# Kernel tuning notes

Measured on AMD Instinct MI355X. Metric: run time of the kernel, lower is better.

Reference implementation:

```python
import jax, jax.numpy as jnp
import numpy as np

EPS = 1e-8
ELASTICITY = jnp.array([0.05, 0.12, 0.08, 0.15, 0.10], dtype=jnp.float32)
N_SIDE = 3  # sqrt(control_points=9)


def _kernel_distance(d2):
    # kornia TPS radial basis: 0.5 * r^2 * log(r^2 + eps)
    return 0.5 * d2 * jnp.log(d2 + EPS)


def _pair_sq_dist(a, b):  # [B,N,2],[B,M,2] -> [B,N,M]
    return jnp.sum((a[:, :, None, :] - b[:, None, :, :]) ** 2, axis=-1)


def grid_sample_bilinear(img, grid):
    """F.grid_sample, mode=bilinear, padding_mode=zeros, align_corners=True.
    img [B,C,H,W], grid [B,H,W,2] with (x,y) in [-1,1]."""
    B, C, H, W = img.shape
    gx = (grid[..., 0] + 1.0) * 0.5 * (W - 1)
    gy = (grid[..., 1] + 1.0) * 0.5 * (H - 1)
    x0 = jnp.floor(gx); y0 = jnp.floor(gy)
    x1 = x0 + 1.0; y1 = y0 + 1.0
    wx1 = gx - x0; wx0 = 1.0 - wx1
    wy1 = gy - y0; wy0 = 1.0 - wy1
    b = jnp.arange(B)[:, None, None]

    def gather(yi, xi):
        valid = (xi >= 0) & (xi <= W - 1) & (yi >= 0) & (yi <= H - 1)
        xc = jnp.clip(xi, 0, W - 1).astype(jnp.int32)
        yc = jnp.clip(yi, 0, H - 1).astype(jnp.int32)
        v = img[b, :, yc, xc]  # [B,H,W,C]
        return v * valid[..., None].astype(img.dtype)

    out = (gather(y0, x0) * (wy0 * wx0)[..., None]
           + gather(y0, x1) * (wy0 * wx1)[..., None]
           + gather(y1, x0) * (wy1 * wx0)[..., None]
           + gather(y1, x1) * (wy1 * wx1)[..., None])
    return jnp.transpose(out, (0, 3, 1, 2))


def control_points_src(B):
    ii, jj = jnp.meshgrid(jnp.arange(N_SIDE, dtype=jnp.float32),
                          jnp.arange(N_SIDE, dtype=jnp.float32), indexing='ij')
    src = jnp.stack([2.0 * ii / (N_SIDE - 1) - 1.0,
                     2.0 * jj / (N_SIDE - 1) - 1.0], axis=-1).reshape(-1, 2)
    return jnp.broadcast_to(src, (B, N_SIDE * N_SIDE, 2))


def point_elasticity(masks_f):
    # masks_f [B,nc,H,W]; 5x5 window around each control point, argmax class
    H, W = masks_f.shape[2], masks_f.shape[3]
    elas = []
    for i in range(N_SIDE):
        for j in range(N_SIDE):
            y = int(i / (N_SIDE - 1) * (H - 1))
            x = int(j / (N_SIDE - 1) * (W - 1))
            y0, y1 = max(0, y - 2), min(H, y + 3)
            x0, x1 = max(0, x - 2), min(W, x + 3)
            region = masks_f[:, :, y0:y1, x0:x1].sum((2, 3))  # [B,nc]
            dom = jnp.argmax(region, axis=1)
            elas.append(ELASTICITY[dom])
    return jnp.stack(elas, axis=1)  # [B,9]


def get_tps_transform(src, dst):
    B, N, _ = src.shape
    K = _kernel_distance(_pair_sq_dist(src, src))                 # [B,N,N]
    P = jnp.concatenate([jnp.ones((B, N, 1), src.dtype), src], -1)  # [B,N,3]
    top = jnp.concatenate([K, P], axis=-1)
    bot = jnp.concatenate([jnp.swapaxes(P, 1, 2),
                           jnp.zeros((B, 3, 3), src.dtype)], axis=-1)
    L = jnp.concatenate([top, bot], axis=1)                        # [B,N+3,N+3]
    rhs = jnp.concatenate([dst, jnp.zeros((B, 3, 2), src.dtype)], axis=1)
    w = jnp.linalg.solve(L, rhs)
    return w[:, :N], w[:, N:]


def warp_image_tps(img, centers, kernel_w, affine_w):
    B, C, H, W = img.shape
    gx, gy = jnp.meshgrid(jnp.linspace(-1.0, 1.0, W), jnp.linspace(-1.0, 1.0, H))
    pts = jnp.stack([gx.ravel(), gy.ravel()], axis=-1)             # [HW,2]
    pts = jnp.broadcast_to(pts, (B, H * W, 2))
    k = _kernel_distance(_pair_sq_dist(pts, centers))              # [B,HW,N]
    pts_aug = jnp.concatenate([jnp.ones((B, H * W, 1), img.dtype), pts], -1)
    warped = k @ kernel_w + pts_aug @ affine_w                     # [B,HW,2]
    return grid_sample_bilinear(img, warped.reshape(B, H, W, 2))


def tps_transform(img, masks_f, noise):
    B = img.shape[0]
    disp = noise * point_elasticity(masks_f)[..., None]            # [B,9,2]
    # smooth the single interior control point (i=j=1 -> idx 4)
    neigh = (disp[:, 1] + disp[:, 7] + disp[:, 3] + disp[:, 5]) * 0.25
    disp = disp.at[:, 4].set(0.8 * disp[:, 4] + 0.2 * neigh)
    src = control_points_src(B)
    kw, aw = get_tps_transform(src, src + disp)
    return warp_image_tps(img, src, kw, aw)


def class_aware_mixup(x, masks_f, lam, perm):
    bg = (masks_f.sum(1, keepdims=True) == 0).astype(x.dtype)
    fg = (masks_f == 1).astype(x.dtype).sum(1, keepdims=True)
    return bg * x + fg * (lam * x + (1.0 - lam) * x[perm])


def setup_inputs() -> dict:
    key = jax.random.key(0)
    k1, k2, k3, k4, k5, k6 = jax.random.split(key, 6)
    B, H, W, NC = 128, 192, 192, 5
    return {
        'x': jax.random.normal(k1, (B, 1, H, W), dtype=jnp.float32),
        'masks': jax.random.randint(k2, (B, NC, H, W), 0, 2, dtype=jnp.int32),
        'lam': jax.random.beta(k3, 0.4, 0.4, dtype=jnp.float32),
        'perm': jax.random.permutation(k4, B).astype(jnp.int32),
        'noise_g': jax.random.normal(k5, (B, 9, 2), dtype=jnp.float32),
        'noise_l': jax.random.normal(k6, (B, 9, 2), dtype=jnp.float32),
        'epoch': 10,
        'total_epochs': 100,
    }


def reference(x, masks, lam, perm, noise_g, noise_l, epoch, total_epochs):
    masks_f = masks.astype(x.dtype)
    mixed_x = class_aware_mixup(x, masks_f, lam, perm)
    global_aug = tps_transform(mixed_x, masks_f, noise_g)
    local_aug = tps_transform(x, masks_f, noise_l)
    return (global_aug, local_aug)
```

## Files before the change

kernel.cpp:

```cpp
#include <hip/hip_runtime.h>
#include <math.h>

#define B_   128
#define H_   192
#define W_   192
#define NC_  5
#define HW_  (H_*W_)
#define NPTS 9
#define EPS_ 1e-8f
#define CHUNK 16

typedef int   vint4   __attribute__((ext_vector_type(4)));
typedef float vfloat4 __attribute__((ext_vector_type(4)));
typedef float vfloat2 __attribute__((ext_vector_type(2)));

struct LinvT { float m[12][NPTS]; };

__global__ __launch_bounds__(256) void mixup_kernel(
    const float* __restrict__ x, const int* __restrict__ masks,
    const float* __restrict__ lam_p, const int* __restrict__ perm,
    float* __restrict__ mixed)
{
    int idx = blockIdx.x * 256 + threadIdx.x;
    const int total4 = B_ * HW_ / 4;
    if (idx >= total4) return;
    float lam = lam_p[0];
    int b  = idx / (HW_ / 4);
    int p4 = (idx - b * (HW_ / 4)) * 4;
    const vfloat4 xv = *reinterpret_cast<const vfloat4*>(x + (size_t)b * HW_ + p4);
    int pb = perm[b];
    const vfloat4 xp = *reinterpret_cast<const vfloat4*>(x + (size_t)pb * HW_ + p4);

    vint4 ma[NC_];
    #pragma unroll
    for (int c = 0; c < NC_; ++c) {
        const vint4* mp = reinterpret_cast<const vint4*>(masks + ((size_t)b * NC_ + c) * HW_ + p4);
        ma[c] = __builtin_nontemporal_load(mp);
    }
    vfloat4 outv;
    #pragma unroll
    for (int l = 0; l < 4; ++l) {
        int s = 0, fg = 0;
        #pragma unroll
        for (int c = 0; c < NC_; ++c) { int m = ma[c][l]; s += m; fg += (m == 1); }
        float bg = (s == 0) ? 1.f : 0.f;
        outv[l] = bg * xv[l] + (float)fg * (lam * xv[l] + (1.f - lam) * xp[l]);
    }
    *reinterpret_cast<vfloat4*>(mixed + (size_t)b * HW_ + p4) = outv;
}

__global__ void prep_kernel(const int* __restrict__ masks,
                            const float* __restrict__ ng,
                            const float* __restrict__ nl,
                            LinvT Linv, float* __restrict__ wts)
{
    const float ETAB[5] = {0.05f, 0.12f, 0.08f, 0.15f, 0.1f};
    __shared__ int   sums[NPTS][NC_];
    __shared__ float elas_s[NPTS];
    int b = blockIdx.x;
    int t = threadIdx.x;

    if (t < NPTS * NC_) {
        int pt = t / NC_, c = t - pt * NC_;
        int i = pt / 3, j = pt % 3;
        int yc = (i * (H_ - 1)) / 2;
        int xc = (j * (W_ - 1)) / 2;
        int y0 = yc - 2 < 0 ? 0 : yc - 2;
        int y1 = yc + 3 > H_ ? H_ : yc + 3;
        int x0 = xc - 2 < 0 ? 0 : xc - 2;
        int x1 = xc + 3 > W_ ? W_ : xc + 3;
        int s = 0;
        for (int y = y0; y < y1; ++y)
            for (int xx = x0; xx < x1; ++xx)
                s += masks[((size_t)b * NC_ + c) * HW_ + y * W_ + xx];
        sums[pt][c] = s;
    }
    __syncthreads();
    if (t < NPTS) {
        int best = -1, best_c = 0;
        #pragma unroll
        for (int c = 0; c < NC_; ++c) {
            int s = sums[t][c];
            if (s > best) { best = s; best_c = c; }
        }
        elas_s[t] = ETAB[best_c];
    }
    __syncthreads();
    if (t < 24) {
        int tr = t / 12, r = t - tr * 12;
        const float* noise = (tr == 0) ? ng : nl;
        float disp[NPTS][2];
        #pragma unroll
        for (int k = 0; k < NPTS; ++k) {
            float e = elas_s[k];
            disp[k][0] = noise[((size_t)b * NPTS + k) * 2 + 0] * e;
            disp[k][1] = noise[((size_t)b * NPTS + k) * 2 + 1] * e;
        }
        #pragma unroll
        for (int c = 0; c < 2; ++c) {
            float nb = (disp[1][c] + disp[7][c] + disp[3][c] + disp[5][c]) * 0.25f;
            disp[4][c] = 0.8f * disp[4][c] + 0.2f * nb;
        }
        float a0 = 0.f, a1 = 0.f;
        #pragma unroll
        for (int k = 0; k < NPTS; ++k) {
            float d0 = (float)(k / 3 - 1) + disp[k][0];
            float d1 = (float)(k % 3 - 1) + disp[k][1];
            a0 += Linv.m[r][k] * d0;
            a1 += Linv.m[r][k] * d1;
        }
        float* wout = wts + ((size_t)tr * B_ + b) * 24;
        wout[r * 2 + 0] = a0;
        wout[r * 2 + 1] = a1;
    }
}

__device__ __forceinline__ void tps_coords_pk(
    const vfloat2* __restrict__ wt2, float px, float py, const float* __restrict__ u,
    int& o00, int& o01, int& o10, int& o11,
    float& w00, float& w01, float& w10, float& w11)
{
    vfloat2 g = wt2[9];
    g = __builtin_elementwise_fma((vfloat2){px, px}, wt2[10], g);
    g = __builtin_elementwise_fma((vfloat2){py, py}, wt2[11], g);
    #pragma unroll
    for (int k = 0; k < NPTS; ++k)
        g = __builtin_elementwise_fma((vfloat2){u[k], u[k]}, wt2[k], g);

    const float sc = 0.5f * (float)(W_ - 1);
    float ix = fmaf(g.x, sc, sc);
    float iy = fmaf(g.y, sc, sc);
    float x0f = floorf(ix), y0f = floorf(iy);
    float wx1 = ix - x0f, wx0 = 1.f - wx1;
    float wy1 = iy - y0f, wy0 = 1.f - wy1;
    int x0 = (int)x0f, y0 = (int)y0f;
    float fx0 = ((unsigned)x0 < 192u)       ? wx0 : 0.f;
    float fx1 = ((unsigned)(x0 + 1) < 192u) ? wx1 : 0.f;
    float fy0 = ((unsigned)y0 < 192u)       ? wy0 : 0.f;
    float fy1 = ((unsigned)(y0 + 1) < 192u) ? wy1 : 0.f;
    w00 = fy0 * fx0; w01 = fy0 * fx1; w10 = fy1 * fx0; w11 = fy1 * fx1;
    int o = y0 * W_ + x0;
    o00 = min(max(o, 0), HW_ - 1);
    o01 = min(max(o + 1, 0), HW_ - 1);
    o10 = min(max(o + W_, 0), HW_ - 1);
    o11 = min(max(o + W_ + 1, 0), HW_ - 1);
}

__global__ __launch_bounds__(256, 2) void warp_kernel(
    const float* __restrict__ x, const float* __restrict__ mixed,
    const float* __restrict__ wts, float* __restrict__ out)
{
    int tx  = threadIdx.x;
    int wpx = blockIdx.x * 64 + (tx & 63);
    int h   = blockIdx.y * 4 + (tx >> 6);
    int p   = h * W_ + wpx;
    float px = -1.f + wpx * (2.f / (float)(W_ - 1));
    float py = -1.f + h   * (2.f / (float)(H_ - 1));

    float u[NPTS];
    #pragma unroll
    for (int k = 0; k < NPTS; ++k) {
        float dx = px - (float)(k / 3 - 1);
        float dy = py - (float)(k % 3 - 1);
        float d2 = dx * dx + dy * dy;
        u[k] = 0.5f * d2 * __logf(d2 + EPS_);
    }

    const vfloat2* wt2base = reinterpret_cast<const vfloat2*>(wts);

    #pragma unroll
    for (int g4 = 0; g4 < CHUNK; g4 += 4) {
        int   o00[4], o01[4], o10[4], o11[4];
        float w00[4], w01[4], w10[4], w11[4];
        const float* src[4];
        #pragma unroll
        for (int q = 0; q < 4; ++q) {
            int combo = blockIdx.z * CHUNK + g4 + q;
            int t = combo >> 7;
            int b = combo & (B_ - 1);
            src[q] = (t == 0 ? mixed : x) + (size_t)b * HW_;
            tps_coords_pk(wt2base + (size_t)combo * 12, px, py, u,
                          o00[q], o01[q], o10[q], o11[q],
                          w00[q], w01[q], w10[q], w11[q]);
        }
        float v00[4], v01[4], v10[4], v11[4];
        #pragma unroll
        for (int q = 0; q < 4; ++q) {
            v00[q] = src[q][o00[q]];
            v01[q] = src[q][o01[q]];
            v10[q] = src[q][o10[q]];
            v11[q] = src[q][o11[q]];
        }
        #pragma unroll
        for (int q = 0; q < 4; ++q) {
            int combo = blockIdx.z * CHUNK + g4 + q;
            float val = w00[q] * v00[q] + w01[q] * v01[q] +
                        w10[q] * v10[q] + w11[q] * v11[q];
            __builtin_nontemporal_store(val, &out[(size_t)combo * HW_ + p]);
        }
    }
}

static void build_linv(LinvT* out)
{
    double srcp[NPTS][2];
    for (int k = 0; k < NPTS; ++k) {
        srcp[k][0] = (double)(k / 3) - 1.0;
        srcp[k][1] = (double)(k % 3) - 1.0;
    }
    double A[12][24];
    for (int r = 0; r < 12; ++r)
        for (int c = 0; c < 24; ++c) A[r][c] = 0.0;
    for (int i = 0; i < NPTS; ++i) {
        for (int j = 0; j < NPTS; ++j) {
            double dx = srcp[i][0] - srcp[j][0];
            double dy = srcp[i][1] - srcp[j][1];
            double d2 = dx * dx + dy * dy;
            A[i][j] = 0.5 * d2 * log(d2 + 1e-8);
        }
        A[i][9]  = 1.0; A[i][10] = srcp[i][0]; A[i][11] = srcp[i][1];
        A[9][i]  = 1.0; A[10][i] = srcp[i][0]; A[11][i] = srcp[i][1];
    }
    for (int r = 0; r < 12; ++r) A[r][12 + r] = 1.0;
    for (int col = 0; col < 12; ++col) {
        int piv = col; double mx = fabs(A[col][col]);
        for (int r = col + 1; r < 12; ++r)
            if (fabs(A[r][col]) > mx) { mx = fabs(A[r][col]); piv = r; }
        if (piv != col)
            for (int c = 0; c < 24; ++c) { double tmp = A[col][c]; A[col][c] = A[piv][c]; A[piv][c] = tmp; }
        double d = A[col][col];
        for (int c = 0; c < 24; ++c) A[col][c] /= d;
        for (int r = 0; r < 12; ++r) {
            if (r == col) continue;
            double f = A[r][col];
            if (f != 0.0)
                for (int c = 0; c < 24; ++c) A[r][c] -= f * A[col][c];
        }
    }
    for (int r = 0; r < 12; ++r)
        for (int k = 0; k < NPTS; ++k)
            out->m[r][k] = (float)A[r][12 + k];
}

extern "C" void kernel_launch(void* const* d_in, const int* in_sizes, int n_in,
                              void* d_out, int out_size, void* d_ws, size_t ws_size,
                              hipStream_t stream)
{
    (void)in_sizes; (void)n_in; (void)out_size; (void)ws_size;
    const float* x     = (const float*)d_in[0];
    const int*   masks = (const int*)d_in[1];
    const float* lam   = (const float*)d_in[2];
    const int*   perm  = (const int*)d_in[3];
    const float* ng    = (const float*)d_in[4];
    const float* nl    = (const float*)d_in[5];
    float* out = (float*)d_out;

    char* ws = (char*)d_ws;
    float* wts   = (float*)ws;
    float* mixed = (float*)(ws + 32768);

    LinvT Linv;
    build_linv(&Linv);

    int total4 = B_ * HW_ / 4;
    mixup_kernel<<<(total4 + 255) / 256, 256, 0, stream>>>(x, masks, lam, perm, mixed);
    prep_kernel<<<B_, 64, 0, stream>>>(masks, ng, nl, Linv, wts);

    dim3 wgrid(W_ / 64, H_ / 4, (2 * B_) / CHUNK);
    warp_kernel<<<wgrid, 256, 0, stream>>>(x, mixed, wts, out);
}
```

Measured before the change: 61.05 us.

## Zero-pad source images so bilinear gather needs no bounds checks

```diff
diff --git a/kernel.cpp b/kernel.cpp
--- a/kernel.cpp
+++ b/kernel.cpp
@@ -1,25 +1,29 @@
 #include <hip/hip_runtime.h>
 #include <math.h>
 
-#define B_   128
-#define H_   192
-#define W_   192
-#define NC_  5
-#define HW_  (H_*W_)
-#define NPTS 9
-#define EPS_ 1e-8f
+#define B_    128
+#define H_    192
+#define W_    192
+#define NC_   5
+#define HW_   (H_*W_)
+#define NPTS  9
+#define EPS_  1e-8f
 #define CHUNK 16
+#define PADW  200
+#define PADH  195
+#define PADSZ (PADH*PADW)
 
 typedef int   vint4   __attribute__((ext_vector_type(4)));
 typedef float vfloat4 __attribute__((ext_vector_type(4)));
 typedef float vfloat2 __attribute__((ext_vector_type(2)));
+typedef float f2a     __attribute__((ext_vector_type(2), aligned(4)));
 
 struct LinvT { float m[12][NPTS]; };
 
-__global__ __launch_bounds__(256) void mixup_kernel(
+__global__ __launch_bounds__(256) void mixup_pad_kernel(
     const float* __restrict__ x, const int* __restrict__ masks,
     const float* __restrict__ lam_p, const int* __restrict__ perm,
-    float* __restrict__ mixed)
+    float* __restrict__ xpad, float* __restrict__ mixpad)
 {
     int idx = blockIdx.x * 256 + threadIdx.x;
     const int total4 = B_ * HW_ / 4;
@@ -27,6 +31,9 @@
     float lam = lam_p[0];
     int b  = idx / (HW_ / 4);
     int p4 = (idx - b * (HW_ / 4)) * 4;
+    int y  = p4 / W_;
+    int x4 = p4 - y * W_;
+
     const vfloat4 xv = *reinterpret_cast<const vfloat4*>(x + (size_t)b * HW_ + p4);
     int pb = perm[b];
     const vfloat4 xp = *reinterpret_cast<const vfloat4*>(x + (size_t)pb * HW_ + p4);
@@ -46,7 +53,44 @@
         float bg = (s == 0) ? 1.f : 0.f;
         outv[l] = bg * xv[l] + (float)fg * (lam * xv[l] + (1.f - lam) * xp[l]);
     }
-    *reinterpret_cast<vfloat4*>(mixed + (size_t)b * HW_ + p4) = outv;
+
+    float* xd = xpad   + (size_t)b * PADSZ;
+    float* md = mixpad + (size_t)b * PADSZ;
+    int io = (y + 1) * PADW + x4 + 4;
+    *reinterpret_cast<vfloat4*>(xd + io) = xv;
+    *reinterpret_cast<vfloat4*>(md + io) = outv;
+
+    const vfloat4 z = {0.f, 0.f, 0.f, 0.f};
+    if (x4 == 0) {
+        *reinterpret_cast<vfloat4*>(xd + io - 4) = z;
+        *reinterpret_cast<vfloat4*>(md + io - 4) = z;
+    }
+    if (x4 == W_ - 4) {
+        *reinterpret_cast<vfloat4*>(xd + io + 4) = z;
+        *reinterpret_cast<vfloat4*>(md + io + 4) = z;
+    }
+    if (y == 0) {
+        *reinterpret_cast<vfloat4*>(xd + io - PADW) = z;
+        *reinterpret_cast<vfloat4*>(md + io - PADW) = z;
+        if (x4 == 0)      { *reinterpret_cast<vfloat4*>(xd + io - PADW - 4) = z;
+                            *reinterpret_cast<vfloat4*>(md + io - PADW - 4) = z; }
+        if (x4 == W_ - 4) { *reinterpret_cast<vfloat4*>(xd + io - PADW + 4) = z;
+                            *reinterpret_cast<vfloat4*>(md + io - PADW + 4) = z; }
+    }
+    if (y == H_ - 1) {
+        *reinterpret_cast<vfloat4*>(xd + io + PADW)     = z;
+        *reinterpret_cast<vfloat4*>(md + io + PADW)     = z;
+        *reinterpret_cast<vfloat4*>(xd + io + 2 * PADW) = z;
+        *reinterpret_cast<vfloat4*>(md + io + 2 * PADW) = z;
+        if (x4 == 0)      { *reinterpret_cast<vfloat4*>(xd + io + PADW - 4) = z;
+                            *reinterpret_cast<vfloat4*>(md + io + PADW - 4) = z;
+                            *reinterpret_cast<vfloat4*>(xd + io + 2 * PADW - 4) = z;
+                            *reinterpret_cast<vfloat4*>(md + io + 2 * PADW - 4) = z; }
+        if (x4 == W_ - 4) { *reinterpret_cast<vfloat4*>(xd + io + PADW + 4) = z;
+                            *reinterpret_cast<vfloat4*>(md + io + PADW + 4) = z;
+                            *reinterpret_cast<vfloat4*>(xd + io + 2 * PADW + 4) = z;
+                            *reinterpret_cast<vfloat4*>(md + io + 2 * PADW + 4) = z; }
+    }
 }
 
 __global__ void prep_kernel(const int* __restrict__ masks,
@@ -115,6 +159,108 @@
     }
 }
 
+__global__ __launch_bounds__(256, 2) void warp_pad_kernel(
+    const float* __restrict__ xpad, const float* __restrict__ mixpad,
+    const float* __restrict__ wts, float* __restrict__ out)
+{
+    int tx  = threadIdx.x;
+    int wpx = blockIdx.x * 64 + (tx & 63);
+    int h   = blockIdx.y * 4 + (tx >> 6);
+    int p   = h * W_ + wpx;
+    float px = -1.f + wpx * (2.f / (float)(W_ - 1));
+    float py = -1.f + h   * (2.f / (float)(H_ - 1));
+
+    float u[NPTS];
+    #pragma unroll
+    for (int k = 0; k < NPTS; ++k) {
+        float dx = px - (float)(k / 3 - 1);
+        float dy = py - (float)(k % 3 - 1);
+        float d2 = dx * dx + dy * dy;
+        u[k] = 0.5f * d2 * __logf(d2 + EPS_);
+    }
+
+    const vfloat2* wt2base = reinterpret_cast<const vfloat2*>(wts);
+
+    #pragma unroll
+    for (int g4 = 0; g4 < CHUNK; g4 += 4) {
+        int     ofs[4];
+        vfloat2 wtop[4], wbot[4];
+        const float* src[4];
+        #pragma unroll
+        for (int q = 0; q < 4; ++q) {
+            int combo = blockIdx.z * CHUNK + g4 + q;
+            int t = combo >> 7;
+            int b = combo & (B_ - 1);
+            src[q] = (t == 0 ? mixpad : xpad) + (size_t)b * PADSZ;
+
+            const vfloat2* wt2 = wt2base + (size_t)combo * 12;
+            vfloat2 g = wt2[9];
+            g = __builtin_elementwise_fma((vfloat2){px, px}, wt2[10], g);
+            g = __builtin_elementwise_fma((vfloat2){py, py}, wt2[11], g);
+            #pragma unroll
+            for (int k = 0; k < NPTS; ++k)
+                g = __builtin_elementwise_fma((vfloat2){u[k], u[k]}, wt2[k], g);
+
+            const float sc = 0.5f * (float)(W_ - 1);
+            vfloat2 ixy = __builtin_elementwise_fma(g, (vfloat2){sc, sc}, (vfloat2){sc, sc});
+            float ix = fminf(fmaxf(ixy.x, -1.f), 192.f);
+            float iy = fminf(fmaxf(ixy.y, -1.f), 192.f);
+            float fx = floorf(ix), fy = floorf(iy);
+            float wx1 = ix - fx, wy1 = iy - fy;
+            float wx0 = 1.f - wx1, wy0 = 1.f - wy1;
+            int x0 = (int)fx, y0 = (int)fy;
+            wtop[q] = (vfloat2){wy0, wy0} * (vfloat2){wx0, wx1};
+            wbot[q] = (vfloat2){wy1, wy1} * (vfloat2){wx0, wx1};
+            ofs[q]  = y0 * PADW + x0;
+        }
+        vfloat2 vt[4], vb[4];
+        #pragma unroll
+        for (int q = 0; q < 4; ++q) {
+            vt[q] = *reinterpret_cast<const f2a*>(src[q] + ofs[q] + (PADW + 4));
+            vb[q] = *reinterpret_cast<const f2a*>(src[q] + ofs[q] + (2 * PADW + 4));
+        }
+        #pragma unroll
+        for (int q = 0; q < 4; ++q) {
+            int combo = blockIdx.z * CHUNK + g4 + q;
+            vfloat2 acc = vt[q] * wtop[q];
+            acc = __builtin_elementwise_fma(vb[q], wbot[q], acc);
+            float val = acc.x + acc.y;
+            __builtin_nontemporal_store(val, &out[(size_t)combo * HW_ + p]);
+        }
+    }
+}
+
+__global__ __launch_bounds__(256) void mixup_kernel(
+    const float* __restrict__ x, const int* __restrict__ masks,
+    const float* __restrict__ lam_p, const int* __restrict__ perm,
+    float* __restrict__ mixed)
+{
+    int idx = blockIdx.x * 256 + threadIdx.x;
+    const int total4 = B_ * HW_ / 4;
+    if (idx >= total4) return;
+    float lam = lam_p[0];
+    int b  = idx / (HW_ / 4);
+    int p4 = (idx - b * (HW_ / 4)) * 4;
+    const vfloat4 xv = *reinterpret_cast<const vfloat4*>(x + (size_t)b * HW_ + p4);
+    int pb = perm[b];
+    const vfloat4 xp = *reinterpret_cast<const vfloat4*>(x + (size_t)pb * HW_ + p4);
+    vint4 ma[NC_];
+    #pragma unroll
+    for (int c = 0; c < NC_; ++c)
+        ma[c] = __builtin_nontemporal_load(
+            reinterpret_cast<const vint4*>(masks + ((size_t)b * NC_ + c) * HW_ + p4));
+    vfloat4 outv;
+    #pragma unroll
+    for (int l = 0; l < 4; ++l) {
+        int s = 0, fg = 0;
+        #pragma unroll
+        for (int c = 0; c < NC_; ++c) { int m = ma[c][l]; s += m; fg += (m == 1); }
+        float bg = (s == 0) ? 1.f : 0.f;
+        outv[l] = bg * xv[l] + (float)fg * (lam * xv[l] + (1.f - lam) * xp[l]);
+    }
+    *reinterpret_cast<vfloat4*>(mixed + (size_t)b * HW_ + p4) = outv;
+}
+
 __device__ __forceinline__ void tps_coords_pk(
     const vfloat2* __restrict__ wt2, float px, float py, const float* __restrict__ u,
     int& o00, int& o01, int& o10, int& o11,
@@ -126,7 +272,6 @@
     #pragma unroll
     for (int k = 0; k < NPTS; ++k)
         g = __builtin_elementwise_fma((vfloat2){u[k], u[k]}, wt2[k], g);
-
     const float sc = 0.5f * (float)(W_ - 1);
     float ix = fmaf(g.x, sc, sc);
     float iy = fmaf(g.y, sc, sc);
@@ -156,7 +301,6 @@
     int p   = h * W_ + wpx;
     float px = -1.f + wpx * (2.f / (float)(W_ - 1));
     float py = -1.f + h   * (2.f / (float)(H_ - 1));
-
     float u[NPTS];
     #pragma unroll
     for (int k = 0; k < NPTS; ++k) {
@@ -165,9 +309,7 @@
         float d2 = dx * dx + dy * dy;
         u[k] = 0.5f * d2 * __logf(d2 + EPS_);
     }
-
     const vfloat2* wt2base = reinterpret_cast<const vfloat2*>(wts);
-
     #pragma unroll
     for (int g4 = 0; g4 < CHUNK; g4 += 4) {
         int   o00[4], o01[4], o10[4], o11[4];
@@ -246,7 +388,7 @@
                               void* d_out, int out_size, void* d_ws, size_t ws_size,
                               hipStream_t stream)
 {
-    (void)in_sizes; (void)n_in; (void)out_size; (void)ws_size;
+    (void)in_sizes; (void)n_in; (void)out_size;
     const float* x     = (const float*)d_in[0];
     const int*   masks = (const int*)d_in[1];
     const float* lam   = (const float*)d_in[2];
@@ -256,16 +398,28 @@
     float* out = (float*)d_out;
 
     char* ws = (char*)d_ws;
-    float* wts   = (float*)ws;
-    float* mixed = (float*)(ws + 32768);
+    float* wts = (float*)ws;
 
     LinvT Linv;
     build_linv(&Linv);
 
+    size_t pad_bytes = (size_t)B_ * PADSZ * sizeof(float);
+    size_t need_pad  = 32768 + 2 * pad_bytes;
+
     int total4 = B_ * HW_ / 4;
-    mixup_kernel<<<(total4 + 255) / 256, 256, 0, stream>>>(x, masks, lam, perm, mixed);
-    prep_kernel<<<B_, 64, 0, stream>>>(masks, ng, nl, Linv, wts);
-
-    dim3 wgrid(W_ / 64, H_ / 4, (2 * B_) / CHUNK);
-    warp_kernel<<<wgrid, 256, 0, stream>>>(x, mixed, wts, out);
-}
+    if (ws_size >= need_pad) {
+        float* xpad   = (float*)(ws + 32768);
+        float* mixpad = (float*)(ws + 32768 + pad_bytes);
+        mixup_pad_kernel<<<(total4 + 255) / 256, 256, 0, stream>>>(
+            x, masks, lam, perm, xpad, mixpad);
+        prep_kernel<<<B_, 64, 0, stream>>>(masks, ng, nl, Linv, wts);
+        dim3 wgrid(W_ / 64, H_ / 4, (2 * B_) / CHUNK);
+        warp_pad_kernel<<<wgrid, 256, 0, stream>>>(xpad, mixpad, wts, out);
+    } else {
+        float* mixed = (float*)(ws + 32768);
+        mixup_kernel<<<(total4 + 255) / 256, 256, 0, stream>>>(x, masks, lam, perm, mixed);
+        prep_kernel<<<B_, 64, 0, stream>>>(masks, ng, nl, Linv, wts);
+        dim3 wgrid(W_ / 64, H_ / 4, (2 * B_) / CHUNK);
+        warp_kernel<<<wgrid, 256, 0, stream>>>(x, mixed, wts, out);
+    }
+}
```

Result: no change. 62.11 us (+1.7%).

## Fuse mixup with local TPS warp in one launch, warp global separately

Applied to the files above, without the earlier changes.

```diff
diff --git a/kernel.cpp b/kernel.cpp
--- a/kernel.cpp
+++ b/kernel.cpp
@@ -1,53 +1,22 @@
 #include <hip/hip_runtime.h>
 #include <math.h>
 
-#define B_   128
-#define H_   192
-#define W_   192
-#define NC_  5
-#define HW_  (H_*W_)
-#define NPTS 9
-#define EPS_ 1e-8f
-#define CHUNK 16
+#define B_    128
+#define H_    192
+#define W_    192
+#define NC_   5
+#define HW_   (H_*W_)
+#define NPTS  9
+#define EPS_  1e-8f
+#define CHUNK 8
+#define MIXB  (B_*HW_/4/256)
+#define LOCB  ((W_/64)*(H_/4)*(B_/CHUNK))
 
 typedef int   vint4   __attribute__((ext_vector_type(4)));
 typedef float vfloat4 __attribute__((ext_vector_type(4)));
 typedef float vfloat2 __attribute__((ext_vector_type(2)));
 
 struct LinvT { float m[12][NPTS]; };
-
-__global__ __launch_bounds__(256) void mixup_kernel(
-    const float* __restrict__ x, const int* __restrict__ masks,
-    const float* __restrict__ lam_p, const int* __restrict__ perm,
-    float* __restrict__ mixed)
-{
-    int idx = blockIdx.x * 256 + threadIdx.x;
-    const int total4 = B_ * HW_ / 4;
-    if (idx >= total4) return;
-    float lam = lam_p[0];
-    int b  = idx / (HW_ / 4);
-    int p4 = (idx - b * (HW_ / 4)) * 4;
-    const vfloat4 xv = *reinterpret_cast<const vfloat4*>(x + (size_t)b * HW_ + p4);
-    int pb = perm[b];
-    const vfloat4 xp = *reinterpret_cast<const vfloat4*>(x + (size_t)pb * HW_ + p4);
-
-    vint4 ma[NC_];
-    #pragma unroll
-    for (int c = 0; c < NC_; ++c) {
-        const vint4* mp = reinterpret_cast<const vint4*>(masks + ((size_t)b * NC_ + c) * HW_ + p4);
-        ma[c] = __builtin_nontemporal_load(mp);
-    }
-    vfloat4 outv;
-    #pragma unroll
-    for (int l = 0; l < 4; ++l) {
-        int s = 0, fg = 0;
-        #pragma unroll
-        for (int c = 0; c < NC_; ++c) { int m = ma[c][l]; s += m; fg += (m == 1); }
-        float bg = (s == 0) ? 1.f : 0.f;
-        outv[l] = bg * xv[l] + (float)fg * (lam * xv[l] + (1.f - lam) * xp[l]);
-    }
-    *reinterpret_cast<vfloat4*>(mixed + (size_t)b * HW_ + p4) = outv;
-}
 
 __global__ void prep_kernel(const int* __restrict__ masks,
                             const float* __restrict__ ng,
@@ -126,7 +95,6 @@
     #pragma unroll
     for (int k = 0; k < NPTS; ++k)
         g = __builtin_elementwise_fma((vfloat2){u[k], u[k]}, wt2[k], g);
-
     const float sc = 0.5f * (float)(W_ - 1);
     float ix = fmaf(g.x, sc, sc);
     float iy = fmaf(g.y, sc, sc);
@@ -146,13 +114,13 @@
     o11 = min(max(o + W_ + 1, 0), HW_ - 1);
 }
 
-__global__ __launch_bounds__(256, 2) void warp_kernel(
-    const float* __restrict__ x, const float* __restrict__ mixed,
-    const float* __restrict__ wts, float* __restrict__ out)
+__device__ __forceinline__ void warp_body(
+    const float* __restrict__ srcb, const float* __restrict__ wts,
+    float* __restrict__ out, int gx, int gy, int combo0)
 {
     int tx  = threadIdx.x;
-    int wpx = blockIdx.x * 64 + (tx & 63);
-    int h   = blockIdx.y * 4 + (tx >> 6);
+    int wpx = gx * 64 + (tx & 63);
+    int h   = gy * 4 + (tx >> 6);
     int p   = h * W_ + wpx;
     float px = -1.f + wpx * (2.f / (float)(W_ - 1));
     float py = -1.f + h   * (2.f / (float)(H_ - 1));
@@ -175,10 +143,9 @@
         const float* src[4];
         #pragma unroll
         for (int q = 0; q < 4; ++q) {
-            int combo = blockIdx.z * CHUNK + g4 + q;
-            int t = combo >> 7;
+            int combo = combo0 + g4 + q;
             int b = combo & (B_ - 1);
-            src[q] = (t == 0 ? mixed : x) + (size_t)b * HW_;
+            src[q] = srcb + (size_t)b * HW_;
             tps_coords_pk(wt2base + (size_t)combo * 12, px, py, u,
                           o00[q], o01[q], o10[q], o11[q],
                           w00[q], w01[q], w10[q], w11[q]);
@@ -193,12 +160,63 @@
         }
         #pragma unroll
         for (int q = 0; q < 4; ++q) {
-            int combo = blockIdx.z * CHUNK + g4 + q;
+            int combo = combo0 + g4 + q;
             float val = w00[q] * v00[q] + w01[q] * v01[q] +
                         w10[q] * v10[q] + w11[q] * v11[q];
             __builtin_nontemporal_store(val, &out[(size_t)combo * HW_ + p]);
         }
     }
+}
+
+__global__ __launch_bounds__(256, 2) void mix_local_kernel(
+    const float* __restrict__ x, const int* __restrict__ masks,
+    const float* __restrict__ lam_p, const int* __restrict__ perm,
+    float* __restrict__ mixed, const float* __restrict__ wts,
+    float* __restrict__ out)
+{
+    int bid   = blockIdx.x;
+    int group = bid / 3;
+    int r     = bid - group * 3;
+
+    if (r < 2) {
+        int mb  = group * 2 + r;
+        int idx = mb * 256 + threadIdx.x;
+        float lam = lam_p[0];
+        int b  = idx / (HW_ / 4);
+        int p4 = (idx - b * (HW_ / 4)) * 4;
+        const vfloat4 xv = *reinterpret_cast<const vfloat4*>(x + (size_t)b * HW_ + p4);
+        int pb = perm[b];
+        const vfloat4 xp = *reinterpret_cast<const vfloat4*>(x + (size_t)pb * HW_ + p4);
+
+        vint4 ma[NC_];
+        #pragma unroll
+        for (int c = 0; c < NC_; ++c)
+            ma[c] = __builtin_nontemporal_load(
+                reinterpret_cast<const vint4*>(masks + ((size_t)b * NC_ + c) * HW_ + p4));
+        vfloat4 outv;
+        #pragma unroll
+        for (int l = 0; l < 4; ++l) {
+            int s = 0, fg = 0;
+            #pragma unroll
+            for (int c = 0; c < NC_; ++c) { int m = ma[c][l]; s += m; fg += (m == 1); }
+            float bg = (s == 0) ? 1.f : 0.f;
+            outv[l] = bg * xv[l] + (float)fg * (lam * xv[l] + (1.f - lam) * xp[l]);
+        }
+        *reinterpret_cast<vfloat4*>(mixed + (size_t)b * HW_ + p4) = outv;
+    } else {
+        int lb = group;
+        int gx = lb % 3;
+        int gy = (lb / 3) % 48;
+        int gz = lb / 144;
+        warp_body(x, wts, out, gx, gy, B_ + gz * CHUNK);
+    }
+}
+
+__global__ __launch_bounds__(256, 2) void warp_global_kernel(
+    const float* __restrict__ mixed, const float* __restrict__ wts,
+    float* __restrict__ out)
+{
+    warp_body(mixed, wts, out, blockIdx.x, blockIdx.y, blockIdx.z * CHUNK);
 }
 
 static void build_linv(LinvT* out)
@@ -262,10 +280,9 @@
     LinvT Linv;
     build_linv(&Linv);
 
-    int total4 = B_ * HW_ / 4;
-    mixup_kernel<<<(total4 + 255) / 256, 256, 0, stream>>>(x, masks, lam, perm, mixed);
     prep_kernel<<<B_, 64, 0, stream>>>(masks, ng, nl, Linv, wts);
-
-    dim3 wgrid(W_ / 64, H_ / 4, (2 * B_) / CHUNK);
-    warp_kernel<<<wgrid, 256, 0, stream>>>(x, mixed, wts, out);
-}
+    mix_local_kernel<<<MIXB + LOCB, 256, 0, stream>>>(
+        x, masks, lam, perm, mixed, wts, out);
+    warp_global_kernel<<<dim3(W_ / 64, H_ / 4, (B_ / CHUNK)), 256, 0, stream>>>(
+        mixed, wts, out);
+}
```

Result: faster. 58.62 us (-4.0%).
